# Performance work log

Measured on AMD Instinct MI355X. Metric: run time of the kernel, lower is better.

## Reference

```python
import jax, jax.numpy as jnp
import numpy as np
from jax import lax

EPS = 1e-5

# int4 fake-quant (Brevitas-style, per-tensor float scale)
# signed act: [-8, 7]; unsigned act: [0, 15]; weight narrow-range: [-7, 7]

def ste_round(x):
    # straight-through round (matches Brevitas STE; forward math == round)
    return x + lax.stop_gradient(jnp.round(x) - x)

def fq(x, s, lo, hi):
    return jnp.clip(ste_round(x / s), lo, hi) * s

def qw(w):
    # Int4WeightQuant: per-tensor scale from max-abs stats, narrow range [-7,7]
    s = jnp.max(jnp.abs(w)) / 7.0
    return jnp.clip(ste_round(w / s), -7.0, 7.0) * s

def conv(x, w, pad):
    return lax.conv_general_dilated(x, w, (1, 1), pad,
                                    dimension_numbers=('NCHW', 'OIHW', 'NCHW'))

def maxpool2(x):
    return lax.reduce_window(x, -jnp.inf, lax.max, (1, 1, 2, 2), (1, 1, 2, 2), 'VALID')

def bn_apply(x, bn):
    g, b, m, v = bn[0], bn[1], bn[2], bn[3]
    inv = g / jnp.sqrt(v + EPS)
    return x * inv[None, :, None, None] + (b - m * inv)[None, :, None, None]

def block(x, w, bn, s_in, s_relu, pool):
    x = fq(x, s_in, -8.0, 7.0)          # conv input_quant (signed int4)
    x = conv(x, qw(w), 'SAME')          # 3x3 quant conv, no bias
    x = bn_apply(x, bn)                 # BatchNorm (eval, running stats)
    x = jax.nn.relu(x)
    x = fq(x, s_relu, 0.0, 15.0)        # QuantReLU (unsigned int4)
    return maxpool2(x) if pool else x

def _forward(x, ws, b9, bns, scales):
    x = fq(x, scales[0], -8.0, 7.0)     # QuantIdentity (signed int4)
    for i in range(8):
        x = block(x, ws[i], bns[i], scales[1 + i], scales[10 + i], pool=(i < 4))
    x = fq(x, scales[9], -8.0, 7.0)     # head input_quant
    x = conv(x, qw(ws[8]), 'VALID') + b9[None, :, None, None]  # 1x1 head with bias
    return x


def setup_inputs() -> dict:
    key = jax.random.key(0)
    ks = jax.random.split(key, 32)
    B, H, W = 16, 320, 640
    x = jax.random.normal(ks[0], (B, 3, H, W), dtype=jnp.float32)
    wshapes = [(16, 3, 3, 3), (32, 16, 3, 3), (64, 32, 3, 3)] + [(64, 64, 3, 3)] * 5 + [(36, 64, 1, 1)]
    inp = {'x': x}
    for i, sh in enumerate(wshapes):
        inp[f'w{i+1}'] = 0.05 * jax.random.normal(ks[1 + i], sh, dtype=jnp.float32)
    inp['b9'] = 0.01 * jax.random.normal(ks[10], (36,), dtype=jnp.float32)
    chans = [16, 32, 64, 64, 64, 64, 64, 64]
    for i, c in enumerate(chans):
        k1, k2, k3, k4 = jax.random.split(ks[11 + i], 4)
        g = 0.75 + 0.5 * jax.random.uniform(k1, (c,), dtype=jnp.float32)
        b = 0.1 * jax.random.normal(k2, (c,), dtype=jnp.float32)
        m = 0.1 * jax.random.normal(k3, (c,), dtype=jnp.float32)
        v = 0.5 + 0.5 * jax.random.uniform(k4, (c,), dtype=jnp.float32)
        inp[f'bn{i+1}'] = jnp.stack([g, b, m, v])  # (4, C)
    inp['scales'] = 0.02 + 0.1 * jax.random.uniform(ks[30], (18,), dtype=jnp.float32)
    return inp


def reference(x, w1, w2, w3, w4, w5, w6, w7, w8, w9, b9,
              bn1, bn2, bn3, bn4, bn5, bn6, bn7, bn8, scales):
    ws = [w1, w2, w3, w4, w5, w6, w7, w8, w9]
    bns = [bn1, bn2, bn3, bn4, bn5, bn6, bn7, bn8]
    return _forward(x, ws, b9, bns, scales)
```

## Files before the change

kernel.cpp:

```cpp
#include <hip/hip_runtime.h>
#include <stdint.h>

#define EPSV 1e-5f

typedef int v4i __attribute__((ext_vector_type(4)));

__device__ __forceinline__ v4i mfma16(v4i a, v4i b, v4i c) {
    return __builtin_amdgcn_mfma_i32_16x16x64_i8(a, b, c, 0, 0, 0);
}

__device__ __forceinline__ int8_t q_epi(int s, float fscale, float inv, float beta,
                                        float s_relu, float s_next)
{
#pragma clang fp contract(off)
    float y = (float)s * fscale;
    y = y * inv;
    y = y + beta;
    float r = rintf(y / s_relu);
    r = fminf(fmaxf(r, 0.f), 15.f);
    float v = r * s_relu;
    float r2 = rintf(v / s_next);
    r2 = fminf(fmaxf(r2, -8.f), 7.f);
    return (int8_t)(int)r2;
}

struct WPtrs { const float* w[9]; int n[9]; };

__global__ __launch_bounds__(256) void k_wmax(WPtrs a, unsigned* __restrict__ smax)
{
    const int t = blockIdx.y;
    const int n = a.n[t];
    const float* w = a.w[t];
    float m = 0.f;
    for (int i = blockIdx.x * 256 + threadIdx.x; i < n; i += 16 * 256)
        m = fmaxf(m, fabsf(w[i]));
#pragma unroll
    for (int off = 32; off > 0; off >>= 1) m = fmaxf(m, __shfl_down(m, off));
    __shared__ float red[4];
    if ((threadIdx.x & 63) == 0) red[threadIdx.x >> 6] = m;
    __syncthreads();
    if (threadIdx.x == 0) {
        m = fmaxf(fmaxf(red[0], red[1]), fmaxf(red[2], red[3]));
        atomicMax(smax + t, __float_as_uint(m));
    }
}

struct PackArgs {
    const float* w[9];
    const float* bn[8];
    const unsigned* smax;
    int* qw;
    float* bnp;
};

#define NB_B    207
#define NB_HEAD 3
#define NB_BN   2

__global__ __launch_bounds__(256) void k_pack(PackArgs a)
{
#pragma clang fp contract(off)
    const int blk = blockIdx.x;
    if (blk < NB_B) {
        const int u = blk * 256 + threadIdx.x;
        const int bcum[9] = {0, 256, 1792, 6912, 16128, 25344, 34560, 43776, 52992};
        const int CIGA[8] = {1, 4, 8, 16, 16, 16, 16, 16};
        const int COA[8]  = {16, 32, 64, 64, 64, 64, 64, 64};
        const int NTA[8]  = {1, 2, 4, 4, 4, 4, 4, 4};
        const int CINA[8] = {3, 16, 32, 64, 64, 64, 64, 64};
        int L = 0;
        while (u >= bcum[L + 1]) ++L;
        const int rem = u - bcum[L];
        const int d = rem & 3;
        const int lane = (rem >> 2) & 63;
        const int gnt = rem >> 8;
        const int NT = NTA[L];
        const int nt = gnt % NT;
        const int g = gnt / NT;
        const int CIG = CIGA[L], CIN = CINA[L], CO = COA[L];
        const int TG = 16 / CIG;
        const int n = nt * 16 + (lane & 15);
        const float s = __uint_as_float(a.smax[L]) / 7.0f;
        const float* w = a.w[L];
        unsigned dw = 0;
        for (int jb = 0; jb < 4; ++jb) {
            const int k = 16 * (lane >> 4) + 4 * d + jb;
            const int tap = g * TG + k / (4 * CIG);
            const int ci = k % (4 * CIG);
            int qv = 0;
            if (tap < 9 && ci < CIN && n < CO) {
                float rr = rintf(w[(n * CIN + ci) * 9 + tap] / s);
                rr = fminf(fmaxf(rr, -7.f), 7.f);
                qv = (int)rr;
            }
            dw |= ((unsigned)(qv & 0xff)) << (8 * jb);
        }
        a.qw[u] = (int)dw;
    } else if (blk < NB_B + NB_HEAD) {
        const int uh = (blk - NB_B) * 256 + threadIdx.x;
        const int d = uh & 3;
        const int lane = (uh >> 2) & 63;
        const int nt = uh >> 8;
        const int n = nt * 16 + (lane & 15);
        const float s = __uint_as_float(a.smax[8]) / 7.0f;
        const float* w = a.w[8];
        unsigned dw = 0;
        for (int jb = 0; jb < 4; ++jb) {
            const int ci = 16 * (lane >> 4) + 4 * d + jb;
            int qv = 0;
            if (n < 36) {
                float rr = rintf(w[n * 64 + ci] / s);
                rr = fminf(fmaxf(rr, -7.f), 7.f);
                qv = (int)rr;
            }
            dw |= ((unsigned)(qv & 0xff)) << (8 * jb);
        }
        a.qw[52992 + uh] = (int)dw;
    } else {
        const int id = (blk - NB_B - NB_HEAD) * 256 + threadIdx.x;
        if (id >= 512) return;
        const int l = id >> 6, c = id & 63;
        const int C[8] = {16, 32, 64, 64, 64, 64, 64, 64};
        if (c < C[l]) {
            const float* bn = a.bn[l];
            const int Cl = C[l];
            float g = bn[c], b = bn[Cl + c], m = bn[2 * Cl + c], v = bn[3 * Cl + c];
            float inv = g / sqrtf(v + EPSV);
            float mi = m * inv;
            a.bnp[l * 128 + c] = inv;
            a.bnp[l * 128 + 64 + c] = b - mi;
        }
    }
}

__global__ __launch_bounds__(256) void k_conv0(
    const float* __restrict__ x, int8_t* __restrict__ out,
    const int* __restrict__ bfrag, const float* __restrict__ scales,
    const unsigned* __restrict__ smax, const float* __restrict__ bnp)
{
#pragma clang fp contract(off)
    __shared__ int tile[660];
    __shared__ float bnl[128];

    const int b = blockIdx.z;
    const int py0 = blockIdx.y * 4;
    const int px0 = blockIdx.x * 32;
    const int ty0 = 2 * py0 - 1;
    const int tx0 = 2 * px0 - 1;
    const float s0 = scales[0], s1 = scales[1];

    for (int i = threadIdx.x; i < 660; i += 256) {
        const int ly = i / 66;
        const int lx = i - ly * 66;
        const int gy = ty0 + ly, gx = tx0 + lx;
        int v = 0;
        if ((unsigned)gy < 320u && (unsigned)gx < 640u) {
#pragma unroll
            for (int ci = 0; ci < 3; ++ci) {
                float xv = x[((size_t)(b * 3 + ci) * 320 + gy) * 640 + gx];
                float r = rintf(xv / s0);
                r = fminf(fmaxf(r, -8.f), 7.f);
                float vv = r * s0;
                float r2 = rintf(vv / s1);
                r2 = fminf(fmaxf(r2, -8.f), 7.f);
                v |= ((int)r2 & 0xff) << (8 * ci);
            }
        }
        tile[i] = v;
    }
    if (threadIdx.x < 128) bnl[threadIdx.x] = bnp[threadIdx.x];

    const int lane = threadIdx.x & 63;
    const int wv = threadIdx.x >> 6;
    const v4i bfv = *(const v4i*)&bfrag[lane * 4];
    __syncthreads();

    const int q = lane >> 4;
    const int m = lane & 15;
    const int px_sub = m >> 2;
    const int op = m & 3;
    const int lyb = 2 * wv + (op >> 1);
    const int lxb0 = 2 * px_sub + (op & 1);

    const float sw = __uint_as_float(smax[0]) / 7.0f;
    const float fscale = scales[1] * sw;
    const float s_relu = scales[10];
    const float s_next = scales[2];
    const float inv = bnl[m];
    const float beta = bnl[64 + m];
    const int py = py0 + wv;

    for (int xs = 0; xs < 8; ++xs) {
        v4i af;
#pragma unroll
        for (int d = 0; d < 4; ++d) {
            int t = 4 * q + d; t = min(t, 8);
            const int ky = (t * 11) >> 5;
            const int kx = t - 3 * ky;
            af[d] = tile[(lyb + ky) * 66 + 8 * xs + lxb0 + kx];
        }
        v4i acc = mfma16(af, bfv, (v4i){0, 0, 0, 0});
        const int px = px0 + 4 * xs + q;
        const int s = max(max(acc[0], acc[1]), max(acc[2], acc[3]));
        out[((size_t)((b * 160 + py) * 320 + px)) * 16 + m] =
            q_epi(s, fscale, inv, beta, s_relu, s_next);
    }
}

template <int CIG, int CO, bool POOL, int H, int W, int XL, int NROWS, bool FUSED>
__global__ __launch_bounds__(256) void k_mconv(
    const int8_t* __restrict__ in, int8_t* __restrict__ out,
    const int* __restrict__ bfrag, const float* __restrict__ scales,
    const unsigned* __restrict__ smax, const float* __restrict__ bnp,
    int layer, int sin_idx, int srelu_idx, int snext_idx,
    const int* __restrict__ hfrag, const float* __restrict__ b9,
    float* __restrict__ dout)
{
    constexpr int NT = CO / 16;
    constexpr int TG = 16 / CIG;
    constexpr int NG = (9 + TG - 1) / TG;
    constexpr int WPR = POOL ? 1 : 2;
    constexpr int NTW = POOL ? NT : NT / 2;
    constexpr int OPW = POOL ? 4 : 16;
    constexpr int S = POOL ? 2 : 1;
    constexpr int TLH = S * NROWS + 2;
    constexpr int TLW = S * OPW * XL + 2;
    constexpr int TILE_DW = TLH * TLW * CIG;
    constexpr bool PRELOAD = (NG * NT <= 8);
    constexpr int Ho = POOL ? H / 2 : H;
    constexpr int Wo = POOL ? W / 2 : W;
    static_assert(WPR * NROWS == 4, "4 waves per block");
    static_assert(POOL || CIG == 16, "nonpool path assumes CIG=16");
    static_assert(!FUSED || (!POOL && XL == 1 && NROWS == 2), "fused head shape");

    __shared__ int tile[TILE_DW];
    __shared__ float bnl[128];
    __shared__ int code_dw[FUSED ? 512 : 1];

    const int b = blockIdx.z;
    const int py0 = blockIdx.y * NROWS;
    const int px0 = blockIdx.x * (OPW * XL);
    const int ty0 = S * py0 - 1;
    const int tx0 = S * px0 - 1;
    const int* gin = (const int*)in;

    for (int i = threadIdx.x; i < TILE_DW; i += 256) {
        const int cig = i & (CIG - 1);
        const int rest = i / CIG;
        const int lx = rest % TLW;
        const int ly = rest / TLW;
        const int gy = ty0 + ly, gx = tx0 + lx;
        int v = 0;
        if ((unsigned)gy < (unsigned)H && (unsigned)gx < (unsigned)W)
            v = gin[((b * H + gy) * W + gx) * CIG + cig];
        tile[i] = v;
    }
    if (threadIdx.x < 128) bnl[threadIdx.x] = bnp[layer * 128 + threadIdx.x];

    const int lane = threadIdx.x & 63;
    const int wv = threadIdx.x >> 6;
    v4i breg[PRELOAD ? NG * NT : 1];
    if constexpr (PRELOAD) {
#pragma unroll
        for (int i = 0; i < NG * NT; ++i)
            breg[i] = *(const v4i*)&bfrag[(i * 64 + lane) * 4];
    }
    __syncthreads();

    const int q = lane >> 4;
    const int m = lane & 15;

    const float swv = __uint_as_float(smax[layer]) / 7.0f;
    const float fscale = scales[sin_idx] * swv;
    const float s_relu = scales[srelu_idx];
    const float s_next = scales[snext_idx];

    int lyb, lxb0, wrow, nt0;
    if (POOL) {
        const int px_sub = m >> 2;
        const int op = m & 3;
        wrow = wv;
        nt0 = 0;
        lyb = 2 * wrow + (op >> 1);
        lxb0 = 2 * px_sub + (op & 1);
    } else {
        wrow = wv >> 1;
        nt0 = (wv & 1) * NTW;
        lyb = wrow;
        lxb0 = m;
    }

    for (int xs = 0; xs < XL; ++xs) {
        v4i acc[NTW];
#pragma unroll
        for (int j = 0; j < NTW; ++j) acc[j] = (v4i){0, 0, 0, 0};

#pragma unroll
        for (int g = 0; g < NG; ++g) {
            v4i af;
            if constexpr (CIG == 16) {
                const int ky = (g * 11) >> 5;
                const int kx = g - 3 * ky;
                int addr;
                if (POOL) addr = ((lyb + ky) * TLW + (8 * xs + lxb0 + kx)) * 16 + 4 * q;
                else      addr = ((lyb + ky) * TLW + (lxb0 + kx)) * 16 + 4 * q;
                af = *(const v4i*)&tile[addr];
            } else if constexpr (CIG == 8) {
                int t = 2 * g + (q >> 1); t = min(t, 8);
                const int ky = (t * 11) >> 5;
                const int kx = t - 3 * ky;
                const int addr = ((lyb + ky) * TLW + (8 * xs + lxb0 + kx)) * 8 + 4 * (q & 1);
                af = *(const v4i*)&tile[addr];
            } else if constexpr (CIG == 4) {
                int t = 4 * g + q; t = min(t, 8);
                const int ky = (t * 11) >> 5;
                const int kx = t - 3 * ky;
                const int addr = ((lyb + ky) * TLW + (8 * xs + lxb0 + kx)) * 4;
                af = *(const v4i*)&tile[addr];
            } else {
#pragma unroll
                for (int d = 0; d < 4; ++d) {
                    int t = 4 * q + d; t = min(t, 8);
                    const int ky = (t * 11) >> 5;
                    const int kx = t - 3 * ky;
                    af[d] = tile[(lyb + ky) * TLW + (8 * xs + lxb0 + kx)];
                }
            }
#pragma unroll
            for (int j = 0; j < NTW; ++j) {
                v4i bf;
                if constexpr (PRELOAD) bf = breg[g * NT + nt0 + j];
                else bf = *(const v4i*)&bfrag[((g * NT + nt0 + j) * 64 + lane) * 4];
                acc[j] = mfma16(af, bf, acc[j]);
            }
        }

        if (POOL) {
            const int py = py0 + wrow;
            const int px = px0 + 4 * xs + q;
            int8_t* po = out + ((size_t)((b * Ho + py) * Wo + px)) * CO + m;
#pragma unroll
            for (int j = 0; j < NTW; ++j) {
                const int co = j * 16 + m;
                const int s = max(max(acc[j][0], acc[j][1]), max(acc[j][2], acc[j][3]));
                po[j * 16] = q_epi(s, fscale, bnl[co], bnl[64 + co], s_relu, s_next);
            }
        } else {
            const int py = py0 + wrow;
#pragma unroll
            for (int j = 0; j < NTW; ++j) {
                const int co = (nt0 + j) * 16 + m;
                const float inv = bnl[co], beta = bnl[64 + co];
#pragma unroll
                for (int r = 0; r < 4; ++r) {
                    const int px = px0 + 4 * q + r;
                    const int8_t cb = q_epi(acc[j][r], fscale, inv, beta, s_relu, s_next);
                    if constexpr (FUSED) {
                        ((int8_t*)code_dw)[(wrow * 16 + 4 * q + r) * 64 + co] = cb;
                    } else {
                        if (px < Wo)
                            out[((size_t)((b * Ho + py) * Wo + px)) * CO + co] = cb;
                    }
                }
            }
        }
    }

    if constexpr (FUSED) {
        __syncthreads();
        if (wv < 2) {
#pragma clang fp contract(off)
            const v4i ha = *(const v4i*)&code_dw[(wv * 16 + m) * 16 + 4 * q];
            const float fs = scales[9] * (__uint_as_float(smax[8]) / 7.0f);
            const int py2 = py0 + wv;
#pragma unroll
            for (int nt = 0; nt < 3; ++nt) {
                const v4i hb = *(const v4i*)&hfrag[(nt * 64 + lane) * 4];
                const v4i hacc = mfma16(ha, hb, (v4i){0, 0, 0, 0});
                const int co = nt * 16 + m;
                if (co < 36) {
                    const float bias = b9[co];
#pragma unroll
                    for (int r = 0; r < 4; ++r) {
                        const int px = px0 + 4 * q + r;
                        if (px < 40) {
                            float y = (float)hacc[r] * fs;
                            dout[((size_t)(b * 36 + co)) * 800 + py2 * 40 + px] = y + bias;
                        }
                    }
                }
            }
        }
    }
}

extern "C" void kernel_launch(void* const* d_in, const int* in_sizes, int n_in,
                              void* d_out, int out_size, void* d_ws, size_t ws_size,
                              hipStream_t stream)
{
    const float* x = (const float*)d_in[0];
    const float* w[9];
    for (int i = 0; i < 9; i++) w[i] = (const float*)d_in[1 + i];
    const float* b9 = (const float*)d_in[10];
    const float* bn[8];
    for (int i = 0; i < 8; i++) bn[i] = (const float*)d_in[11 + i];
    const float* scales = (const float*)d_in[19];

    int8_t* base = (int8_t*)d_ws;
    int8_t* bufA = base;
    int8_t* bufB = base + 13107200;
    int*     qw  = (int*)(base + 26214400);
    unsigned* smax = (unsigned*)(base + 26429440);
    float*   bnp = (float*)(base + 26429952);

    static const int wn[9] = {432, 4608, 18432, 36864, 36864, 36864, 36864, 36864, 2304};
    static const int bo[8] = {0, 256, 1792, 6912, 16128, 25344, 34560, 43776};

    hipMemsetAsync(smax, 0, 9 * sizeof(unsigned), stream);

    WPtrs wp;
    for (int i = 0; i < 9; i++) { wp.w[i] = w[i]; wp.n[i] = wn[i]; }
    k_wmax<<<dim3(16, 9), 256, 0, stream>>>(wp, smax);

    PackArgs pa;
    for (int i = 0; i < 9; i++) pa.w[i] = w[i];
    for (int i = 0; i < 8; i++) pa.bn[i] = bn[i];
    pa.smax = smax; pa.qw = qw; pa.bnp = bnp;
    k_pack<<<NB_B + NB_HEAD + NB_BN, 256, 0, stream>>>(pa);

    k_conv0<<<dim3(10, 40, 16), 256, 0, stream>>>(
        x, bufB, qw + bo[0], scales, smax, bnp);

    k_mconv<4, 32, true, 160, 320, 4, 4, false><<<dim3(10, 20, 16), 256, 0, stream>>>(
        bufB, bufA, qw + bo[1], scales, smax, bnp, 1, 2, 11, 3, nullptr, nullptr, nullptr);
    k_mconv<8, 64, true, 80, 160, 2, 4, false><<<dim3(10, 10, 16), 256, 0, stream>>>(
        bufA, bufB, qw + bo[2], scales, smax, bnp, 2, 3, 12, 4, nullptr, nullptr, nullptr);
    k_mconv<16, 64, true, 40, 80, 1, 4, false><<<dim3(10, 5, 16), 256, 0, stream>>>(
        bufB, bufA, qw + bo[3], scales, smax, bnp, 3, 4, 13, 5, nullptr, nullptr, nullptr);
    k_mconv<16, 64, false, 20, 40, 1, 2, false><<<dim3(3, 10, 16), 256, 0, stream>>>(
        bufA, bufB, qw + bo[4], scales, smax, bnp, 4, 5, 14, 6, nullptr, nullptr, nullptr);
    k_mconv<16, 64, false, 20, 40, 1, 2, false><<<dim3(3, 10, 16), 256, 0, stream>>>(
        bufB, bufA, qw + bo[5], scales, smax, bnp, 5, 6, 15, 7, nullptr, nullptr, nullptr);
    k_mconv<16, 64, false, 20, 40, 1, 2, false><<<dim3(3, 10, 16), 256, 0, stream>>>(
        bufA, bufB, qw + bo[6], scales, smax, bnp, 6, 7, 16, 8, nullptr, nullptr, nullptr);
    k_mconv<16, 64, false, 20, 40, 1, 2, true><<<dim3(3, 10, 16), 256, 0, stream>>>(
        bufB, bufA, qw + bo[7], scales, smax, bnp, 7, 8, 17, 9,
        qw + 52992, b9, (float*)d_out);

    (void)in_sizes; (void)n_in; (void)out_size; (void)ws_size;
}
```

Baseline: 211.4 us.

## Fuse last four convs and head into per-image LDS kernel; LUT requant

The four non-pooling 3x3 layers and the 1x1 head now run in a single kernel with one 1024-thread block per image. Activations ping-pong between two LDS buffers and each layer's weights are staged into LDS, which removes four launches and the global round-trips between those layers. The ReLU-quant to next-input requantisation is replaced by a 16-entry int8 lookup table built in the pack kernel. Pooled layers that do not preload weights into registers now stage them in LDS first. The tail kernel launches only 16 blocks and uses roughly 157 KB of LDS, so it leaves most CUs idle.

```diff
diff --git a/kernel.cpp b/kernel.cpp
--- a/kernel.cpp
+++ b/kernel.cpp
@@ -9,8 +9,8 @@
     return __builtin_amdgcn_mfma_i32_16x16x64_i8(a, b, c, 0, 0, 0);
 }
 
-__device__ __forceinline__ int8_t q_epi(int s, float fscale, float inv, float beta,
-                                        float s_relu, float s_next)
+__device__ __forceinline__ int q_r(int s, float fscale, float inv, float beta,
+                                   float s_relu)
 {
 #pragma clang fp contract(off)
     float y = (float)s * fscale;
@@ -18,10 +18,7 @@
     y = y + beta;
     float r = rintf(y / s_relu);
     r = fminf(fmaxf(r, 0.f), 15.f);
-    float v = r * s_relu;
-    float r2 = rintf(v / s_next);
-    r2 = fminf(fmaxf(r2, -8.f), 7.f);
-    return (int8_t)(int)r2;
+    return (int)r;
 }
 
 struct WPtrs { const float* w[9]; int n[9]; };
@@ -48,14 +45,16 @@
 struct PackArgs {
     const float* w[9];
     const float* bn[8];
+    const float* sc;
     const unsigned* smax;
     int* qw;
     float* bnp;
+    int8_t* lut;
 };
 
 #define NB_B    207
 #define NB_HEAD 3
-#define NB_BN   2
+#define NB_BN   3
 
 __global__ __launch_bounds__(256) void k_pack(PackArgs a)
 {
@@ -118,17 +117,32 @@
         a.qw[52992 + uh] = (int)dw;
     } else {
         const int id = (blk - NB_B - NB_HEAD) * 256 + threadIdx.x;
-        if (id >= 512) return;
-        const int l = id >> 6, c = id & 63;
-        const int C[8] = {16, 32, 64, 64, 64, 64, 64, 64};
-        if (c < C[l]) {
-            const float* bn = a.bn[l];
-            const int Cl = C[l];
-            float g = bn[c], b = bn[Cl + c], m = bn[2 * Cl + c], v = bn[3 * Cl + c];
-            float inv = g / sqrtf(v + EPSV);
-            float mi = m * inv;
-            a.bnp[l * 128 + c] = inv;
-            a.bnp[l * 128 + 64 + c] = b - mi;
+        if (id < 512) {
+            const int l = id >> 6, c = id & 63;
+            const int C[8] = {16, 32, 64, 64, 64, 64, 64, 64};
+            if (c < C[l]) {
+                const float* bn = a.bn[l];
+                const int Cl = C[l];
+                float g = bn[c], b = bn[Cl + c], m = bn[2 * Cl + c], v = bn[3 * Cl + c];
+                float inv = g / sqrtf(v + EPSV);
+                float mi = m * inv;
+                a.bnp[l * 128 + c] = inv;
+                a.bnp[l * 128 + 64 + c] = b - mi;
+            }
+        } else if (id < 656) {
+            const int j = id - 512;
+            const int l = j >> 4, r = j & 15;
+            float code;
+            if (l < 8) {
+                const float s_relu = a.sc[10 + l];
+                const float s_next = (l < 7) ? a.sc[2 + l] : a.sc[9];
+                const float v = (float)r * s_relu;
+                code = fminf(fmaxf(rintf(v / s_next), -8.f), 7.f);
+            } else {
+                const float v = (float)(r - 8) * a.sc[0];
+                code = fminf(fmaxf(rintf(v / a.sc[1]), -8.f), 7.f);
+            }
+            a.lut[j] = (int8_t)(int)code;
         }
     }
 }
@@ -136,18 +150,25 @@
 __global__ __launch_bounds__(256) void k_conv0(
     const float* __restrict__ x, int8_t* __restrict__ out,
     const int* __restrict__ bfrag, const float* __restrict__ scales,
-    const unsigned* __restrict__ smax, const float* __restrict__ bnp)
+    const unsigned* __restrict__ smax, const float* __restrict__ bnp,
+    const int8_t* __restrict__ luts)
 {
 #pragma clang fp contract(off)
     __shared__ int tile[660];
     __shared__ float bnl[128];
+    __shared__ int8_t lc[32];
 
     const int b = blockIdx.z;
     const int py0 = blockIdx.y * 4;
     const int px0 = blockIdx.x * 32;
     const int ty0 = 2 * py0 - 1;
     const int tx0 = 2 * px0 - 1;
-    const float s0 = scales[0], s1 = scales[1];
+    const float s0 = scales[0];
+
+    if (threadIdx.x < 16) lc[threadIdx.x] = luts[threadIdx.x];
+    else if (threadIdx.x < 32) lc[threadIdx.x] = luts[128 + threadIdx.x - 16];
+    if (threadIdx.x < 128) bnl[threadIdx.x] = bnp[threadIdx.x];
+    __syncthreads();
 
     for (int i = threadIdx.x; i < 660; i += 256) {
         const int ly = i / 66;
@@ -160,15 +181,11 @@
                 float xv = x[((size_t)(b * 3 + ci) * 320 + gy) * 640 + gx];
                 float r = rintf(xv / s0);
                 r = fminf(fmaxf(r, -8.f), 7.f);
-                float vv = r * s0;
-                float r2 = rintf(vv / s1);
-                r2 = fminf(fmaxf(r2, -8.f), 7.f);
-                v |= ((int)r2 & 0xff) << (8 * ci);
+                v |= ((int)lc[16 + (int)r + 8] & 0xff) << (8 * ci);
             }
         }
         tile[i] = v;
     }
-    if (threadIdx.x < 128) bnl[threadIdx.x] = bnp[threadIdx.x];
 
     const int lane = threadIdx.x & 63;
     const int wv = threadIdx.x >> 6;
@@ -185,7 +202,6 @@
     const float sw = __uint_as_float(smax[0]) / 7.0f;
     const float fscale = scales[1] * sw;
     const float s_relu = scales[10];
-    const float s_next = scales[2];
     const float inv = bnl[m];
     const float beta = bnl[64 + m];
     const int py = py0 + wv;
@@ -202,46 +218,38 @@
         v4i acc = mfma16(af, bfv, (v4i){0, 0, 0, 0});
         const int px = px0 + 4 * xs + q;
         const int s = max(max(acc[0], acc[1]), max(acc[2], acc[3]));
-        out[((size_t)((b * 160 + py) * 320 + px)) * 16 + m] =
-            q_epi(s, fscale, inv, beta, s_relu, s_next);
-    }
-}
-
-template <int CIG, int CO, bool POOL, int H, int W, int XL, int NROWS, bool FUSED>
+        const int ri = q_r(s, fscale, inv, beta, s_relu);
+        out[((size_t)((b * 160 + py) * 320 + px)) * 16 + m] = lc[ri];
+    }
+}
+
+template <int CIG, int CO, int H, int W, int XL>
 __global__ __launch_bounds__(256) void k_mconv(
     const int8_t* __restrict__ in, int8_t* __restrict__ out,
     const int* __restrict__ bfrag, const float* __restrict__ scales,
     const unsigned* __restrict__ smax, const float* __restrict__ bnp,
-    int layer, int sin_idx, int srelu_idx, int snext_idx,
-    const int* __restrict__ hfrag, const float* __restrict__ b9,
-    float* __restrict__ dout)
-{
+    const int8_t* __restrict__ luts, int layer, int sin_idx, int srelu_idx)
+{
+#pragma clang fp contract(off)
     constexpr int NT = CO / 16;
     constexpr int TG = 16 / CIG;
     constexpr int NG = (9 + TG - 1) / TG;
-    constexpr int WPR = POOL ? 1 : 2;
-    constexpr int NTW = POOL ? NT : NT / 2;
-    constexpr int OPW = POOL ? 4 : 16;
-    constexpr int S = POOL ? 2 : 1;
-    constexpr int TLH = S * NROWS + 2;
-    constexpr int TLW = S * OPW * XL + 2;
+    constexpr int TLH = 2 * 4 + 2;
+    constexpr int TLW = 2 * 4 * XL + 2;
     constexpr int TILE_DW = TLH * TLW * CIG;
     constexpr bool PRELOAD = (NG * NT <= 8);
-    constexpr int Ho = POOL ? H / 2 : H;
-    constexpr int Wo = POOL ? W / 2 : W;
-    static_assert(WPR * NROWS == 4, "4 waves per block");
-    static_assert(POOL || CIG == 16, "nonpool path assumes CIG=16");
-    static_assert(!FUSED || (!POOL && XL == 1 && NROWS == 2), "fused head shape");
+    constexpr int Ho = H / 2, Wo = W / 2;
 
     __shared__ int tile[TILE_DW];
     __shared__ float bnl[128];
-    __shared__ int code_dw[FUSED ? 512 : 1];
+    __shared__ int8_t lsh[16];
+    __shared__ int bsh[PRELOAD ? 1 : NG * NT * 256];
 
     const int b = blockIdx.z;
-    const int py0 = blockIdx.y * NROWS;
-    const int px0 = blockIdx.x * (OPW * XL);
-    const int ty0 = S * py0 - 1;
-    const int tx0 = S * px0 - 1;
+    const int py0 = blockIdx.y * 4;
+    const int px0 = blockIdx.x * (4 * XL);
+    const int ty0 = 2 * py0 - 1;
+    const int tx0 = 2 * px0 - 1;
     const int* gin = (const int*)in;
 
     for (int i = threadIdx.x; i < TILE_DW; i += 256) {
@@ -256,6 +264,11 @@
         tile[i] = v;
     }
     if (threadIdx.x < 128) bnl[threadIdx.x] = bnp[layer * 128 + threadIdx.x];
+    if (threadIdx.x >= 128 && threadIdx.x < 144)
+        lsh[threadIdx.x - 128] = luts[layer * 16 + threadIdx.x - 128];
+    if constexpr (!PRELOAD) {
+        for (int i = threadIdx.x; i < NG * NT * 256; i += 256) bsh[i] = bfrag[i];
+    }
 
     const int lane = threadIdx.x & 63;
     const int wv = threadIdx.x >> 6;
@@ -273,27 +286,17 @@
     const float swv = __uint_as_float(smax[layer]) / 7.0f;
     const float fscale = scales[sin_idx] * swv;
     const float s_relu = scales[srelu_idx];
-    const float s_next = scales[snext_idx];
-
-    int lyb, lxb0, wrow, nt0;
-    if (POOL) {
-        const int px_sub = m >> 2;
-        const int op = m & 3;
-        wrow = wv;
-        nt0 = 0;
-        lyb = 2 * wrow + (op >> 1);
-        lxb0 = 2 * px_sub + (op & 1);
-    } else {
-        wrow = wv >> 1;
-        nt0 = (wv & 1) * NTW;
-        lyb = wrow;
-        lxb0 = m;
-    }
+
+    const int px_sub = m >> 2;
+    const int op = m & 3;
+    const int lyb = 2 * wv + (op >> 1);
+    const int lxb0 = 2 * px_sub + (op & 1);
+    const int py = py0 + wv;
 
     for (int xs = 0; xs < XL; ++xs) {
-        v4i acc[NTW];
-#pragma unroll
-        for (int j = 0; j < NTW; ++j) acc[j] = (v4i){0, 0, 0, 0};
+        v4i acc[NT];
+#pragma unroll
+        for (int j = 0; j < NT; ++j) acc[j] = (v4i){0, 0, 0, 0};
 
 #pragma unroll
         for (int g = 0; g < NG; ++g) {
@@ -301,9 +304,7 @@
             if constexpr (CIG == 16) {
                 const int ky = (g * 11) >> 5;
                 const int kx = g - 3 * ky;
-                int addr;
-                if (POOL) addr = ((lyb + ky) * TLW + (8 * xs + lxb0 + kx)) * 16 + 4 * q;
-                else      addr = ((lyb + ky) * TLW + (lxb0 + kx)) * 16 + 4 * q;
+                const int addr = ((lyb + ky) * TLW + (8 * xs + lxb0 + kx)) * 16 + 4 * q;
                 af = *(const v4i*)&tile[addr];
             } else if constexpr (CIG == 8) {
                 int t = 2 * g + (q >> 1); t = min(t, 8);
@@ -311,68 +312,128 @@
                 const int kx = t - 3 * ky;
                 const int addr = ((lyb + ky) * TLW + (8 * xs + lxb0 + kx)) * 8 + 4 * (q & 1);
                 af = *(const v4i*)&tile[addr];
-            } else if constexpr (CIG == 4) {
+            } else {
                 int t = 4 * g + q; t = min(t, 8);
                 const int ky = (t * 11) >> 5;
                 const int kx = t - 3 * ky;
                 const int addr = ((lyb + ky) * TLW + (8 * xs + lxb0 + kx)) * 4;
                 af = *(const v4i*)&tile[addr];
-            } else {
-#pragma unroll
-                for (int d = 0; d < 4; ++d) {
-                    int t = 4 * q + d; t = min(t, 8);
-                    const int ky = (t * 11) >> 5;
-                    const int kx = t - 3 * ky;
-                    af[d] = tile[(lyb + ky) * TLW + (8 * xs + lxb0 + kx)];
+            }
+#pragma unroll
+            for (int j = 0; j < NT; ++j) {
+                v4i bf;
+                if constexpr (PRELOAD) bf = breg[g * NT + j];
+                else bf = *(const v4i*)&bsh[((g * NT + j) * 64 + lane) * 4];
+                acc[j] = mfma16(af, bf, acc[j]);
+            }
+        }
+
+        const int px = px0 + 4 * xs + q;
+        int8_t* po = out + ((size_t)((b * Ho + py) * Wo + px)) * CO + m;
+#pragma unroll
+        for (int j = 0; j < NT; ++j) {
+            const int co = j * 16 + m;
+            const int s = max(max(acc[j][0], acc[j][1]), max(acc[j][2], acc[j][3]));
+            const int ri = q_r(s, fscale, bnl[co], bnl[64 + co], s_relu);
+            po[j * 16] = lsh[ri];
+        }
+    }
+}
+
+__global__ __launch_bounds__(1024) void k_tail(
+    const int8_t* __restrict__ in, const int* __restrict__ qw,
+    const float* __restrict__ scales, const unsigned* __restrict__ smax,
+    const float* __restrict__ bnp, const int8_t* __restrict__ luts,
+    const int* __restrict__ hfrag, const float* __restrict__ b9,
+    float* __restrict__ dout)
+{
+#pragma clang fp contract(off)
+    __shared__ int8_t img[2][22 * 42 * 64];
+    __shared__ int bsh[9216];
+    __shared__ float bnl[512];
+    __shared__ int8_t lsh[64];
+
+    const int b = blockIdx.x;
+    const int tid = threadIdx.x;
+    const int lane = tid & 63;
+    const int wv = tid >> 6;
+    const int q = lane >> 4;
+    const int m = lane & 15;
+
+    int* ia = (int*)img;
+    for (int i = tid; i < 2 * 22 * 42 * 16; i += 1024) ia[i] = 0;
+    for (int i = tid; i < 512; i += 1024) bnl[i] = bnp[512 + i];
+    if (tid < 64) lsh[tid] = luts[64 + tid];
+    __syncthreads();
+
+    const int* gin = (const int*)in;
+    int* i0 = (int*)img[0];
+    for (int i = tid; i < 12800; i += 1024) {
+        const int c = i & 15;
+        const int px = (i >> 4) % 40;
+        const int y = (i >> 4) / 40;
+        i0[((y + 1) * 42 + px + 1) * 16 + c] = gin[((b * 20 + y) * 40 + px) * 16 + c];
+    }
+
+    const int bo_[4] = {16128, 25344, 34560, 43776};
+    int cur = 0;
+    for (int l = 0; l < 4; ++l) {
+        __syncthreads();
+        const int bofs = bo_[l];
+        for (int i = tid; i < 9216; i += 1024) bsh[i] = qw[bofs + i];
+        __syncthreads();
+
+        const float swv = __uint_as_float(smax[4 + l]) / 7.0f;
+        const float fscale = scales[5 + l] * swv;
+        const float s_relu = scales[14 + l];
+        const int8_t* imin = img[cur];
+        int8_t* imout = img[cur ^ 1];
+
+        for (int it = wv; it < 60; it += 16) {
+            const int y = it / 3;
+            const int st = it - 3 * y;
+            const int pa = st * 16 + m;
+            v4i acc[4];
+#pragma unroll
+            for (int j = 0; j < 4; ++j) acc[j] = (v4i){0, 0, 0, 0};
+#pragma unroll
+            for (int g = 0; g < 9; ++g) {
+                const int ky = (g * 11) >> 5;
+                const int kx = g - 3 * ky;
+                const v4i af = *(const v4i*)&imin[(((y + ky) * 42) + pa + kx) * 64 + 16 * q];
+#pragma unroll
+                for (int j = 0; j < 4; ++j) {
+                    const v4i bf = *(const v4i*)&bsh[((g * 4 + j) * 64 + lane) * 4];
+                    acc[j] = mfma16(af, bf, acc[j]);
                 }
             }
 #pragma unroll
-            for (int j = 0; j < NTW; ++j) {
-                v4i bf;
-                if constexpr (PRELOAD) bf = breg[g * NT + nt0 + j];
-                else bf = *(const v4i*)&bfrag[((g * NT + nt0 + j) * 64 + lane) * 4];
-                acc[j] = mfma16(af, bf, acc[j]);
-            }
-        }
-
-        if (POOL) {
-            const int py = py0 + wrow;
-            const int px = px0 + 4 * xs + q;
-            int8_t* po = out + ((size_t)((b * Ho + py) * Wo + px)) * CO + m;
-#pragma unroll
-            for (int j = 0; j < NTW; ++j) {
+            for (int j = 0; j < 4; ++j) {
                 const int co = j * 16 + m;
-                const int s = max(max(acc[j][0], acc[j][1]), max(acc[j][2], acc[j][3]));
-                po[j * 16] = q_epi(s, fscale, bnl[co], bnl[64 + co], s_relu, s_next);
-            }
-        } else {
-            const int py = py0 + wrow;
-#pragma unroll
-            for (int j = 0; j < NTW; ++j) {
-                const int co = (nt0 + j) * 16 + m;
-                const float inv = bnl[co], beta = bnl[64 + co];
+                const float inv = bnl[l * 128 + co];
+                const float beta = bnl[l * 128 + 64 + co];
 #pragma unroll
                 for (int r = 0; r < 4; ++r) {
-                    const int px = px0 + 4 * q + r;
-                    const int8_t cb = q_epi(acc[j][r], fscale, inv, beta, s_relu, s_next);
-                    if constexpr (FUSED) {
-                        ((int8_t*)code_dw)[(wrow * 16 + 4 * q + r) * 64 + co] = cb;
-                    } else {
-                        if (px < Wo)
-                            out[((size_t)((b * Ho + py) * Wo + px)) * CO + co] = cb;
+                    const int px = st * 16 + 4 * q + r;
+                    if (px < 40) {
+                        const int ri = q_r(acc[j][r], fscale, inv, beta, s_relu);
+                        imout[((y + 1) * 42 + px + 1) * 64 + co] = lsh[l * 16 + ri];
                     }
                 }
             }
         }
-    }
-
-    if constexpr (FUSED) {
-        __syncthreads();
-        if (wv < 2) {
-#pragma clang fp contract(off)
-            const v4i ha = *(const v4i*)&code_dw[(wv * 16 + m) * 16 + 4 * q];
-            const float fs = scales[9] * (__uint_as_float(smax[8]) / 7.0f);
-            const int py2 = py0 + wv;
+        cur ^= 1;
+    }
+    __syncthreads();
+
+    {
+        const float fs = scales[9] * (__uint_as_float(smax[8]) / 7.0f);
+        const int8_t* imin = img[cur];
+        for (int it = wv; it < 60; it += 16) {
+            const int y = it / 3;
+            const int st = it - 3 * y;
+            const int pa = st * 16 + m;
+            const v4i ha = *(const v4i*)&imin[((y + 1) * 42 + pa + 1) * 64 + 16 * q];
 #pragma unroll
             for (int nt = 0; nt < 3; ++nt) {
                 const v4i hb = *(const v4i*)&hfrag[(nt * 64 + lane) * 4];
@@ -382,10 +443,10 @@
                     const float bias = b9[co];
 #pragma unroll
                     for (int r = 0; r < 4; ++r) {
-                        const int px = px0 + 4 * q + r;
+                        const int px = st * 16 + 4 * q + r;
                         if (px < 40) {
-                            float y = (float)hacc[r] * fs;
-                            dout[((size_t)(b * 36 + co)) * 800 + py2 * 40 + px] = y + bias;
+                            float yv = (float)hacc[r] * fs;
+                            dout[((size_t)(b * 36 + co)) * 800 + y * 40 + px] = yv + bias;
                         }
                     }
                 }
@@ -412,9 +473,9 @@
     int*     qw  = (int*)(base + 26214400);
     unsigned* smax = (unsigned*)(base + 26429440);
     float*   bnp = (float*)(base + 26429952);
+    int8_t*  luts = base + 26434048;
 
     static const int wn[9] = {432, 4608, 18432, 36864, 36864, 36864, 36864, 36864, 2304};
-    static const int bo[8] = {0, 256, 1792, 6912, 16128, 25344, 34560, 43776};
 
     hipMemsetAsync(smax, 0, 9 * sizeof(unsigned), stream);
 
@@ -425,27 +486,21 @@
     PackArgs pa;
     for (int i = 0; i < 9; i++) pa.w[i] = w[i];
     for (int i = 0; i < 8; i++) pa.bn[i] = bn[i];
-    pa.smax = smax; pa.qw = qw; pa.bnp = bnp;
+    pa.sc = scales; pa.smax = smax; pa.qw = qw; pa.bnp = bnp; pa.lut = luts;
     k_pack<<<NB_B + NB_HEAD + NB_BN, 256, 0, stream>>>(pa);
 
     k_conv0<<<dim3(10, 40, 16), 256, 0, stream>>>(
-        x, bufB, qw + bo[0], scales, smax, bnp);
-
-    k_mconv<4, 32, true, 160, 320, 4, 4, false><<<dim3(10, 20, 16), 256, 0, stream>>>(
-        bufB, bufA, qw + bo[1], scales, smax, bnp, 1, 2, 11, 3, nullptr, nullptr, nullptr);
-    k_mconv<8, 64, true, 80, 160, 2, 4, false><<<dim3(10, 10, 16), 256, 0, stream>>>(
-        bufA, bufB, qw + bo[2], scales, smax, bnp, 2, 3, 12, 4, nullptr, nullptr, nullptr);
-    k_mconv<16, 64, true, 40, 80, 1, 4, false><<<dim3(10, 5, 16), 256, 0, stream>>>(
-        bufB, bufA, qw + bo[3], scales, smax, bnp, 3, 4, 13, 5, nullptr, nullptr, nullptr);
-    k_mconv<16, 64, false, 20, 40, 1, 2, false><<<dim3(3, 10, 16), 256, 0, stream>>>(
-        bufA, bufB, qw + bo[4], scales, smax, bnp, 4, 5, 14, 6, nullptr, nullptr, nullptr);
-    k_mconv<16, 64, false, 20, 40, 1, 2, false><<<dim3(3, 10, 16), 256, 0, stream>>>(
-        bufB, bufA, qw + bo[5], scales, smax, bnp, 5, 6, 15, 7, nullptr, nullptr, nullptr);
-    k_mconv<16, 64, false, 20, 40, 1, 2, false><<<dim3(3, 10, 16), 256, 0, stream>>>(
-        bufA, bufB, qw + bo[6], scales, smax, bnp, 6, 7, 16, 8, nullptr, nullptr, nullptr);
-    k_mconv<16, 64, false, 20, 40, 1, 2, true><<<dim3(3, 10, 16), 256, 0, stream>>>(
-        bufB, bufA, qw + bo[7], scales, smax, bnp, 7, 8, 17, 9,
-        qw + 52992, b9, (float*)d_out);
+        x, bufB, qw, scales, smax, bnp, luts);
+
+    k_mconv<4, 32, 160, 320, 4><<<dim3(10, 20, 16), 256, 0, stream>>>(
+        bufB, bufA, qw + 256, scales, smax, bnp, luts, 1, 2, 11);
+    k_mconv<8, 64, 80, 160, 2><<<dim3(10, 10, 16), 256, 0, stream>>>(
+        bufA, bufB, qw + 1792, scales, smax, bnp, luts, 2, 3, 12);
+    k_mconv<16, 64, 40, 80, 1><<<dim3(10, 5, 16), 256, 0, stream>>>(
+        bufB, bufA, qw + 6912, scales, smax, bnp, luts, 3, 4, 13);
+
+    k_tail<<<16, 1024, 0, stream>>>(
+        bufA, qw, scales, smax, bnp, luts, qw + 52992, b9, (float*)d_out);
 
     (void)in_sizes; (void)n_in; (void)out_size; (void)ws_size;
 }
```

Measured after the change: 361.4 us. 1.71x slower.
